# Kernel optimization log

Hardware: AMD Instinct MI355X
Metric: run time of the kernel (lower is better)

Reference implementation:

```python
import jax, jax.numpy as jnp
import numpy as np

HIDDEN = 1024
TILE = 128


def setup_inputs() -> dict:
    key = jax.random.key(0)
    ks = jax.random.split(key, 9)
    B, S, D = 2, 4096, HIDDEN
    s = 1.0 / np.sqrt(D)
    return {
        "batch": jax.random.normal(ks[0], (B, S, D), jnp.float32),
        "Wq": jax.random.normal(ks[1], (D, D), jnp.float32) * s,
        "bq": jax.random.normal(ks[2], (D,), jnp.float32) * 0.01,
        "Wk": jax.random.normal(ks[3], (D, D), jnp.float32) * s,
        "bk": jax.random.normal(ks[4], (D,), jnp.float32) * 0.01,
        "Wv": jax.random.normal(ks[5], (D, D), jnp.float32) * s,
        "bv": jax.random.normal(ks[6], (D,), jnp.float32) * 0.01,
        "Wo": jax.random.normal(ks[7], (D, D), jnp.float32) * s,
        "bo": jax.random.normal(ks[8], (D,), jnp.float32) * 0.01,
    }


def reference(batch, Wq, bq, Wk, bk, Wv, bv, Wo, bo):
    B, S, D = batch.shape
    scale = 1.0 / np.sqrt(D)
    T = S // TILE  # seq_len chosen divisible by tile size

    # Projections (nn.Linear: x @ W.T + b)
    q = batch @ Wq.T + bq
    k = batch @ Wk.T + bk
    v = batch @ Wv.T + bv

    # Tile K/V along the sequence axis: [B, T, TILE, D]
    k_t = k.reshape(B, T, TILE, D)
    v_t = v.reshape(B, T, TILE, D)

    # Per-tile scores and per-tile softmax (NOT a global softmax —
    # faithful to the module, which normalizes within each kv tile).
    scores = jnp.einsum("bqd,btkd->btqk", q, k_t) * scale  # [B, T, S, TILE]
    w = jax.nn.softmax(scores, axis=-1)

    # Sum of per-tile attention outputs over kv tiles
    out = jnp.einsum("btqk,btkd->bqd", w, v_t)  # [B, S, D]

    # Normalizing factor: sum of per-tile softmax weights (== T analytically,
    # computed explicitly to match the original math bit-for-bit in spirit)
    norm = w.sum(axis=-1).sum(axis=1)[..., None]  # [B, S, 1]
    out = out / (norm + 1e-6)

    return out @ Wo.T + bo
```

## Files before the change

kernel.cpp:

```cpp
#include <hip/hip_runtime.h>


#define D_ 1024
#define S_ 4096
#define B_ 2

typedef unsigned short u16;
typedef float f32x4 __attribute__((ext_vector_type(4)));
typedef float float4v __attribute__((ext_vector_type(4)));
typedef __bf16 bf16x8 __attribute__((ext_vector_type(8)));
typedef unsigned short us8 __attribute__((ext_vector_type(8)));

static __device__ __forceinline__ u16 f2bf(float f) {
    unsigned int u = __builtin_bit_cast(unsigned int, f);
    u += 0x7FFFu + ((u >> 16) & 1u);
    return (u16)(u >> 16);
}

static __device__ __forceinline__ void gld16(const u16* g, u16* l) {
    __builtin_amdgcn_global_load_lds(
        (const __attribute__((address_space(1))) void*)g,
        (__attribute__((address_space(3))) void*)l, 16, 0, 0);
}

__global__ void cast_kernel(const float* __restrict__ in, u16* __restrict__ out, int n8) {
    int i = blockIdx.x * blockDim.x + threadIdx.x;
    int stride = gridDim.x * blockDim.x;
    for (; i < n8; i += stride) {
        const float4v* p = (const float4v*)in + 2 * (size_t)i;
        float4v a = p[0], b = p[1];
        us8 o;
        o[0] = f2bf(a[0]); o[1] = f2bf(a[1]); o[2] = f2bf(a[2]); o[3] = f2bf(a[3]);
        o[4] = f2bf(b[0]); o[5] = f2bf(b[1]); o[6] = f2bf(b[2]); o[7] = f2bf(b[3]);
        *((us8*)out + i) = o;
    }
}

__global__ void cast4_kernel(const float* __restrict__ w0, const float* __restrict__ w1,
                             const float* __restrict__ w2, const float* __restrict__ w3,
                             u16* __restrict__ out, int n8per) {
    const float* srcs[4] = {w0, w1, w2, w3};
    const float* in = srcs[blockIdx.y];
    u16* o = out + (size_t)blockIdx.y * (size_t)n8per * 8;
    int i = blockIdx.x * blockDim.x + threadIdx.x;
    int stride = gridDim.x * blockDim.x;
    for (; i < n8per; i += stride) {
        const float4v* p = (const float4v*)in + 2 * (size_t)i;
        float4v a = p[0], b = p[1];
        us8 v;
        v[0] = f2bf(a[0]); v[1] = f2bf(a[1]); v[2] = f2bf(a[2]); v[3] = f2bf(a[3]);
        v[4] = f2bf(b[0]); v[5] = f2bf(b[1]); v[6] = f2bf(b[2]); v[7] = f2bf(b[3]);
        *((us8*)o + i) = v;
    }
}

__global__ void transpose_v(const u16* __restrict__ V, u16* __restrict__ Vt) {
    __shared__ u16 t[64][72];
    const int tid = threadIdx.x;
    const int d0 = blockIdx.x * 64;
    const int s0 = blockIdx.y * 64;
    const u16* Vb = V + (size_t)blockIdx.z * ((size_t)S_ * D_);
    u16* Vtb = Vt + (size_t)blockIdx.z * ((size_t)D_ * S_);
#pragma unroll
    for (int it = 0; it < 2; it++) {
        int idx = it * 256 + tid;
        int row = idx >> 3;
        int ch = idx & 7;
        us8 v = *(const us8*)&Vb[(size_t)(s0 + row) * D_ + d0 + ch * 8];
        *(us8*)&t[row][ch * 8] = v;
    }
    __syncthreads();
#pragma unroll
    for (int it = 0; it < 2; it++) {
        int idx = it * 256 + tid;
        int jj = idx >> 3;
        int ch = idx & 7;
        us8 v;
#pragma unroll
        for (int e = 0; e < 8; e++) v[e] = t[ch * 8 + e][jj];
        *(us8*)&Vtb[(size_t)(d0 + jj) * S_ + s0 + ch * 8] = v;
    }
}

template <int EPI>
__global__ __launch_bounds__(256, 2) void gemm_bt(
    const u16* __restrict__ A, const u16* __restrict__ B, void* __restrict__ Cv,
    const float* __restrict__ bias, int K, int lda, int ldb, int ldc,
    long sA, long sB, long sC, float scale)
{
    __shared__ u16 lA[128 * 32];
    __shared__ u16 lB[128 * 32];
    const int tid = threadIdx.x;
    const int lane = tid & 63;
    const int wid = tid >> 6;
    const int wr = wid >> 1, wc = wid & 1;
    const int z = blockIdx.z;
    A += (size_t)z * sA;
    B += (size_t)z * sB;
    const int m0 = blockIdx.y * 128;
    const int n0 = blockIdx.x * 128;

    f32x4 acc[4][4];
#pragma unroll
    for (int i = 0; i < 4; i++)
#pragma unroll
        for (int j = 0; j < 4; j++)
#pragma unroll
            for (int r = 0; r < 4; r++) acc[i][j][r] = 0.0f;

    const int ar = lane & 15;
    const int ak = (lane >> 4) * 8;
    const int srow = tid >> 2;
    const int scol = (tid & 3) * 8;
    const u16* ga = A + (size_t)(m0 + srow) * lda + scol;
    const u16* gb = B + (size_t)(n0 + srow) * ldb + scol;

    for (int k0 = 0; k0 < K; k0 += 32) {
        gld16(ga + k0, &lA[tid * 8]);
        gld16(ga + k0 + (size_t)64 * lda, &lA[2048 + tid * 8]);
        gld16(gb + k0, &lB[tid * 8]);
        gld16(gb + k0 + (size_t)64 * ldb, &lB[2048 + tid * 8]);
        __syncthreads();
        bf16x8 afr[4], bfr[4];
#pragma unroll
        for (int mi = 0; mi < 4; mi++)
            afr[mi] = *(const bf16x8*)&lA[(wr * 64 + mi * 16 + ar) * 32 + ak];
#pragma unroll
        for (int ni = 0; ni < 4; ni++)
            bfr[ni] = *(const bf16x8*)&lB[(wc * 64 + ni * 16 + ar) * 32 + ak];
#pragma unroll
        for (int mi = 0; mi < 4; mi++)
#pragma unroll
            for (int ni = 0; ni < 4; ni++)
                acc[mi][ni] = __builtin_amdgcn_mfma_f32_16x16x32_bf16(
                    afr[mi], bfr[ni], acc[mi][ni], 0, 0, 0);
        __syncthreads();
    }

    const int rr = (lane >> 4) * 4;
    const int cc = lane & 15;
#pragma unroll
    for (int mi = 0; mi < 4; mi++) {
#pragma unroll
        for (int ni = 0; ni < 4; ni++) {
            const int col = n0 + wc * 64 + ni * 16 + cc;
            const int rowb = m0 + wr * 64 + mi * 16 + rr;
            if constexpr (EPI == 0) {
                u16* C = (u16*)Cv + (size_t)z * sC;
                const float bv = bias[col];
#pragma unroll
                for (int r = 0; r < 4; r++)
                    C[(size_t)(rowb + r) * ldc + col] = f2bf(acc[mi][ni][r] + bv);
            } else if constexpr (EPI == 1) {
                u16* C = (u16*)Cv + (size_t)z * sC;
#pragma unroll
                for (int r = 0; r < 4; r++)
                    C[(size_t)(rowb + r) * ldc + col] = f2bf(acc[mi][ni][r] * scale);
            } else {
                float* C = (float*)Cv + (size_t)z * sC;
                const float bv = bias[col];
#pragma unroll
                for (int r = 0; r < 4; r++)
                    C[(size_t)(rowb + r) * ldc + col] = acc[mi][ni][r] + bv;
            }
        }
    }
}

__global__ __launch_bounds__(256, 2) void gemm_scores(
    const u16* __restrict__ Q, const u16* __restrict__ Kmat, u16* __restrict__ W,
    int K, int lda, int ldb, int ldc, long sQ, long sK, long sW)
{
    __shared__ u16 lA[128 * 32];
    __shared__ u16 lB[128 * 32];
    const int tid = threadIdx.x;
    const int lane = tid & 63;
    const int wid = tid >> 6;
    const int z = blockIdx.z;
    const u16* Aq = Q + (size_t)z * sQ;
    const u16* Bk = Kmat + (size_t)z * sK;
    const int m0 = blockIdx.y * 128;
    const int n0 = blockIdx.x * 128;

    f32x4 acc[2][8];
#pragma unroll
    for (int i = 0; i < 2; i++)
#pragma unroll
        for (int j = 0; j < 8; j++)
#pragma unroll
            for (int r = 0; r < 4; r++) acc[i][j][r] = 0.0f;

    const int ar = lane & 15;
    const int ak = (lane >> 4) * 8;
    const int srow = tid >> 2;
    const int scol = (tid & 3) * 8;
    const u16* ga = Aq + (size_t)(m0 + srow) * lda + scol;
    const u16* gb = Bk + (size_t)(n0 + srow) * ldb + scol;

    for (int k0 = 0; k0 < K; k0 += 32) {
        gld16(ga + k0, &lA[tid * 8]);
        gld16(ga + k0 + (size_t)64 * lda, &lA[2048 + tid * 8]);
        gld16(gb + k0, &lB[tid * 8]);
        gld16(gb + k0 + (size_t)64 * ldb, &lB[2048 + tid * 8]);
        __syncthreads();
        bf16x8 afr[2], bfr[8];
#pragma unroll
        for (int mi = 0; mi < 2; mi++)
            afr[mi] = *(const bf16x8*)&lA[(wid * 32 + mi * 16 + ar) * 32 + ak];
#pragma unroll
        for (int ni = 0; ni < 8; ni++)
            bfr[ni] = *(const bf16x8*)&lB[(ni * 16 + ar) * 32 + ak];
#pragma unroll
        for (int mi = 0; mi < 2; mi++)
#pragma unroll
            for (int ni = 0; ni < 8; ni++)
                acc[mi][ni] = __builtin_amdgcn_mfma_f32_16x16x32_bf16(
                    afr[mi], bfr[ni], acc[mi][ni], 0, 0, 0);
        __syncthreads();
    }

    const float SL = 0.03125f * 1.44269504088896341f;
    const int g4 = (lane >> 4) * 4;
    const int cc = lane & 15;
    u16* Wp = W + (size_t)z * sW;
#pragma unroll
    for (int mi = 0; mi < 2; mi++) {
#pragma unroll
        for (int r = 0; r < 4; r++) {
            float m = acc[mi][0][r];
#pragma unroll
            for (int ni = 1; ni < 8; ni++) m = fmaxf(m, acc[mi][ni][r]);
            m = fmaxf(m, __shfl_xor(m, 1));
            m = fmaxf(m, __shfl_xor(m, 2));
            m = fmaxf(m, __shfl_xor(m, 4));
            m = fmaxf(m, __shfl_xor(m, 8));
            float e[8], s = 0.0f;
#pragma unroll
            for (int ni = 0; ni < 8; ni++) {
                e[ni] = exp2f((acc[mi][ni][r] - m) * SL);
                s += e[ni];
            }
            s += __shfl_xor(s, 1);
            s += __shfl_xor(s, 2);
            s += __shfl_xor(s, 4);
            s += __shfl_xor(s, 8);
            const float inv = 1.0f / s;
            const int row = m0 + wid * 32 + mi * 16 + g4 + r;
#pragma unroll
            for (int ni = 0; ni < 8; ni++)
                Wp[(size_t)row * ldc + n0 + ni * 16 + cc] = f2bf(e[ni] * inv);
        }
    }
}

extern "C" void kernel_launch(void* const* d_in, const int* in_sizes, int n_in,
                              void* d_out, int out_size, void* d_ws, size_t ws_size,
                              hipStream_t stream)
{
    const float* X  = (const float*)d_in[0];
    const float* Wq = (const float*)d_in[1];
    const float* bq = (const float*)d_in[2];
    const float* Wk = (const float*)d_in[3];
    const float* bk = (const float*)d_in[4];
    const float* Wv = (const float*)d_in[5];
    const float* bv = (const float*)d_in[6];
    const float* Wo = (const float*)d_in[7];
    const float* bo = (const float*)d_in[8];
    float* OUT = (float*)d_out;

    u16* ws = (u16*)d_ws;
    const size_t NTOK = (size_t)B_ * S_;
    const size_t XSZ = NTOK * D_;
    u16* Xb  = ws;
    u16* Qb  = Xb + XSZ;
    u16* Kb  = Qb + XSZ;
    u16* Vb  = Kb + XSZ;
    u16* Vt  = Vb + XSZ;
    u16* Wqb = Vt + XSZ;
    u16* Wkb = Wqb + (size_t)D_ * D_;
    u16* Wvb = Wkb + (size_t)D_ * D_;
    u16* Wob = Wvb + (size_t)D_ * D_;
    u16* Wsm = Wob + (size_t)D_ * D_;
    u16* Ob  = Xb;

    cast_kernel<<<dim3(2048), dim3(256), 0, stream>>>(X, Xb, (int)(XSZ / 8));
    cast4_kernel<<<dim3(512, 4), dim3(256), 0, stream>>>(Wq, Wk, Wv, Wo, Wqb,
                                                         (int)((size_t)D_ * D_ / 8));

    dim3 gp(D_ / 128, NTOK / 128, 1);
    gemm_bt<0><<<gp, 256, 0, stream>>>(Xb, Wqb, Qb, bq, D_, D_, D_, D_, 0, 0, 0, 1.0f);
    gemm_bt<0><<<gp, 256, 0, stream>>>(Xb, Wkb, Kb, bk, D_, D_, D_, D_, 0, 0, 0, 1.0f);
    gemm_bt<0><<<gp, 256, 0, stream>>>(Xb, Wvb, Vb, bv, D_, D_, D_, D_, 0, 0, 0, 1.0f);

    transpose_v<<<dim3(D_ / 64, S_ / 64, B_), 256, 0, stream>>>(Vb, Vt);

    gemm_scores<<<dim3(S_ / 128, S_ / 128, B_), 256, 0, stream>>>(
        Qb, Kb, Wsm, D_, D_, D_, S_, (long)S_ * D_, (long)S_ * D_, (long)S_ * S_);

    gemm_bt<1><<<dim3(D_ / 128, S_ / 128, B_), 256, 0, stream>>>(
        Wsm, Vt, Ob, nullptr, S_, S_, S_, D_,
        (long)S_ * S_, (long)D_ * S_, (long)S_ * D_, 1.0f / (32.0f + 1e-6f));

    gemm_bt<2><<<dim3(D_ / 128, NTOK / 128, 1), 256, 0, stream>>>(
        Ob, Wob, OUT, bo, D_, D_, D_, D_, 0, 0, 0, 1.0f);
}
```

Before: 417.5 us.

## Fuse QKV projections into one GEMM and remap blocks across XCDs

The three Q/K/V projection GEMMs become a single GEMM against the concatenated weight matrix. It writes an interleaved QKV buffer with row stride 3*D, using a bias vector concatenated by a small new kernel. All GEMMs also remap block indices so that groups of consecutive workgroups (assumed to land on the same XCD) cover neighbouring row tiles, for better L2 reuse. The aims are fewer launches, a larger grid for the projection, and better cache locality. The cost is strided Q/K/V accesses and an extra tiny kernel, and the remap assumes gridDim.y is divisible by 8.

```diff
diff --git a/kernel.cpp b/kernel.cpp
--- a/kernel.cpp
+++ b/kernel.cpp
@@ -21,6 +21,16 @@
     __builtin_amdgcn_global_load_lds(
         (const __attribute__((address_space(1))) void*)g,
         (__attribute__((address_space(3))) void*)l, 16, 0, 0);
+}
+
+static __device__ __forceinline__ void xcd_map(int& bx, int& by) {
+    const int gx = gridDim.x, gy = gridDim.y;
+    int lin = blockIdx.x + blockIdx.y * gx;
+    int ry = gy >> 3;
+    int idx = lin >> 3;
+    int q = idx / ry;
+    bx = q;
+    by = (lin & 7) * ry + (idx - q * ry);
 }
 
 __global__ void cast_kernel(const float* __restrict__ in, u16* __restrict__ out, int n8) {
@@ -54,19 +64,26 @@
     }
 }
 
-__global__ void transpose_v(const u16* __restrict__ V, u16* __restrict__ Vt) {
+__global__ void concat_bias(const float* __restrict__ b0, const float* __restrict__ b1,
+                            const float* __restrict__ b2, float* __restrict__ out) {
+    int i = blockIdx.x * 256 + threadIdx.x;
+    const float* s = (i < 1024) ? b0 : ((i < 2048) ? b1 : b2);
+    out[i] = s[i & 1023];
+}
+
+__global__ void transpose_v(const u16* __restrict__ V, u16* __restrict__ Vt, int ldv) {
     __shared__ u16 t[64][72];
     const int tid = threadIdx.x;
     const int d0 = blockIdx.x * 64;
     const int s0 = blockIdx.y * 64;
-    const u16* Vb = V + (size_t)blockIdx.z * ((size_t)S_ * D_);
+    const u16* Vb = V + (size_t)blockIdx.z * ((size_t)S_ * ldv);
     u16* Vtb = Vt + (size_t)blockIdx.z * ((size_t)D_ * S_);
 #pragma unroll
     for (int it = 0; it < 2; it++) {
         int idx = it * 256 + tid;
         int row = idx >> 3;
         int ch = idx & 7;
-        us8 v = *(const us8*)&Vb[(size_t)(s0 + row) * D_ + d0 + ch * 8];
+        us8 v = *(const us8*)&Vb[(size_t)(s0 + row) * ldv + d0 + ch * 8];
         *(us8*)&t[row][ch * 8] = v;
     }
     __syncthreads();
@@ -97,8 +114,10 @@
     const int z = blockIdx.z;
     A += (size_t)z * sA;
     B += (size_t)z * sB;
-    const int m0 = blockIdx.y * 128;
-    const int n0 = blockIdx.x * 128;
+    int bx, by;
+    xcd_map(bx, by);
+    const int m0 = by * 128;
+    const int n0 = bx * 128;
 
     f32x4 acc[4][4];
 #pragma unroll
@@ -179,8 +198,10 @@
     const int z = blockIdx.z;
     const u16* Aq = Q + (size_t)z * sQ;
     const u16* Bk = Kmat + (size_t)z * sK;
-    const int m0 = blockIdx.y * 128;
-    const int n0 = blockIdx.x * 128;
+    int bx, by;
+    xcd_map(bx, by);
+    const int m0 = by * 128;
+    const int n0 = bx * 128;
 
     f32x4 acc[2][8];
 #pragma unroll
@@ -271,36 +292,37 @@
     u16* ws = (u16*)d_ws;
     const size_t NTOK = (size_t)B_ * S_;
     const size_t XSZ = NTOK * D_;
-    u16* Xb  = ws;
-    u16* Qb  = Xb + XSZ;
-    u16* Kb  = Qb + XSZ;
-    u16* Vb  = Kb + XSZ;
-    u16* Vt  = Vb + XSZ;
-    u16* Wqb = Vt + XSZ;
-    u16* Wkb = Wqb + (size_t)D_ * D_;
-    u16* Wvb = Wkb + (size_t)D_ * D_;
-    u16* Wob = Wvb + (size_t)D_ * D_;
-    u16* Wsm = Wob + (size_t)D_ * D_;
-    u16* Ob  = Xb;
+    u16* Xb   = ws;
+    u16* QKVb = Xb + XSZ;
+    u16* Vt   = QKVb + NTOK * (size_t)(3 * D_);
+    u16* Wqb  = Vt + XSZ;
+    u16* Wsm  = Wqb + (size_t)4 * D_ * D_;
+    float* bqkv = (float*)(Wsm + (size_t)B_ * S_ * S_);
+    u16* Ob   = Xb;
+
+    u16* Qp = QKVb;
+    u16* Kp = QKVb + D_;
+    u16* Vp = QKVb + 2 * D_;
+    const int ldqkv = 3 * D_;
 
     cast_kernel<<<dim3(2048), dim3(256), 0, stream>>>(X, Xb, (int)(XSZ / 8));
     cast4_kernel<<<dim3(512, 4), dim3(256), 0, stream>>>(Wq, Wk, Wv, Wo, Wqb,
                                                          (int)((size_t)D_ * D_ / 8));
-
-    dim3 gp(D_ / 128, NTOK / 128, 1);
-    gemm_bt<0><<<gp, 256, 0, stream>>>(Xb, Wqb, Qb, bq, D_, D_, D_, D_, 0, 0, 0, 1.0f);
-    gemm_bt<0><<<gp, 256, 0, stream>>>(Xb, Wkb, Kb, bk, D_, D_, D_, D_, 0, 0, 0, 1.0f);
-    gemm_bt<0><<<gp, 256, 0, stream>>>(Xb, Wvb, Vb, bv, D_, D_, D_, D_, 0, 0, 0, 1.0f);
-
-    transpose_v<<<dim3(D_ / 64, S_ / 64, B_), 256, 0, stream>>>(Vb, Vt);
+    concat_bias<<<dim3(12), dim3(256), 0, stream>>>(bq, bk, bv, bqkv);
+
+    gemm_bt<0><<<dim3(3 * D_ / 128, NTOK / 128, 1), 256, 0, stream>>>(
+        Xb, Wqb, QKVb, bqkv, D_, D_, D_, ldqkv, 0, 0, 0, 1.0f);
+
+    transpose_v<<<dim3(D_ / 64, S_ / 64, B_), 256, 0, stream>>>(Vp, Vt, ldqkv);
 
     gemm_scores<<<dim3(S_ / 128, S_ / 128, B_), 256, 0, stream>>>(
-        Qb, Kb, Wsm, D_, D_, D_, S_, (long)S_ * D_, (long)S_ * D_, (long)S_ * S_);
+        Qp, Kp, Wsm, D_, ldqkv, ldqkv, S_,
+        (long)S_ * ldqkv, (long)S_ * ldqkv, (long)S_ * S_);
 
     gemm_bt<1><<<dim3(D_ / 128, S_ / 128, B_), 256, 0, stream>>>(
         Wsm, Vt, Ob, nullptr, S_, S_, S_, D_,
         (long)S_ * S_, (long)D_ * S_, (long)S_ * D_, 1.0f / (32.0f + 1e-6f));
 
     gemm_bt<2><<<dim3(D_ / 128, NTOK / 128, 1), 256, 0, stream>>>(
-        Ob, Wob, OUT, bo, D_, D_, D_, D_, 0, 0, 0, 1.0f);
-}
+        Ob, Wqb + (size_t)3 * D_ * D_, OUT, bo, D_, D_, D_, D_, 0, 0, 0, 1.0f);
+}
```

Result: faster. 405.1 us (-3.0%).
